# Kernel optimization log

Measured on AMD Instinct MI355X. Metric: run time of the kernel, lower is better.

## Reference

```python
import jax, jax.numpy as jnp
import numpy as np

N = 50000          # nodes
E_RAND = 800000    # random edges (avg degree 16)
IN, HID, HEADS, OUT = 256, 64, 4, 40
NEG_SLOPE = 0.2    # PyG GATConv default leaky_relu slope
BN_EPS = 1e-5


def setup_inputs() -> dict:
    key = jax.random.key(0)
    ks = jax.random.split(key, 24)
    x = jax.random.normal(ks[0], (N, IN), jnp.float32)
    ei = jax.random.randint(ks[1], (2, E_RAND), 0, N)
    loops = jnp.arange(N, dtype=ei.dtype)
    edge_index = jnp.concatenate([ei, jnp.stack([loops, loops])], axis=1)  # add self loops (PyG default)
    s = 0.1
    d = {
        "x": x,
        "edge_index": edge_index,
        "W0": jax.random.normal(ks[2], (IN, HEADS * HID), jnp.float32) * s,
        "a_src0": jax.random.normal(ks[3], (HEADS, HID), jnp.float32) * s,
        "a_dst0": jax.random.normal(ks[4], (HEADS, HID), jnp.float32) * s,
        "b0": jax.random.normal(ks[5], (HEADS * HID,), jnp.float32) * s,
        "bn0_g": jnp.ones((HEADS * HID,), jnp.float32),
        "bn0_b": jnp.zeros((HEADS * HID,), jnp.float32),
        "bn0_m": jax.random.normal(ks[6], (HEADS * HID,), jnp.float32) * s,
        "bn0_v": jax.random.uniform(ks[7], (HEADS * HID,), jnp.float32, 0.5, 1.5),
        "W1": jax.random.normal(ks[8], (HEADS * HID, HEADS * HID), jnp.float32) * s,
        "a_src1": jax.random.normal(ks[9], (HEADS, HID), jnp.float32) * s,
        "a_dst1": jax.random.normal(ks[10], (HEADS, HID), jnp.float32) * s,
        "b1": jax.random.normal(ks[11], (HEADS * HID,), jnp.float32) * s,
        "bn1_g": jnp.ones((HEADS * HID,), jnp.float32),
        "bn1_b": jnp.zeros((HEADS * HID,), jnp.float32),
        "bn1_m": jax.random.normal(ks[12], (HEADS * HID,), jnp.float32) * s,
        "bn1_v": jax.random.uniform(ks[13], (HEADS * HID,), jnp.float32, 0.5, 1.5),
        "W2": jax.random.normal(ks[14], (HEADS * HID, OUT), jnp.float32) * s,
        "a_src2": jax.random.normal(ks[15], (1, OUT), jnp.float32) * s,
        "a_dst2": jax.random.normal(ks[16], (1, OUT), jnp.float32) * s,
        "b2": jax.random.normal(ks[17], (OUT,), jnp.float32) * s,
    }
    return d


def gat_conv(x, edge_index, W, att_src, att_dst, heads, ch):
    """PyG GATConv (eval mode): gather -> leaky_relu attn -> segment softmax -> scatter add."""
    src, dst = edge_index[0], edge_index[1]
    h = (x @ W).reshape(-1, heads, ch)                       # [N,H,C]
    a_s = jnp.einsum('nhc,hc->nh', h, att_src)
    a_d = jnp.einsum('nhc,hc->nh', h, att_dst)
    e = jax.nn.leaky_relu(a_s[src] + a_d[dst], NEG_SLOPE)    # [E,H]
    m = jax.ops.segment_max(e, dst, num_segments=N)
    m = jax.lax.stop_gradient(jnp.where(jnp.isfinite(m), m, 0.0))
    p = jnp.exp(e - m[dst])
    denom = jax.ops.segment_sum(p, dst, num_segments=N)
    alpha = p / (denom[dst] + 1e-16)                         # [E,H]
    msg = h[src] * alpha[:, :, None]                         # [E,H,C]
    return jax.ops.segment_sum(msg, dst, num_segments=N)     # [N,H,C]


def _bn(h, g, b, m, v):
    return g * (h - m) * jax.lax.rsqrt(v + BN_EPS) + b


def reference(x, edge_index, W0, a_src0, a_dst0, b0, bn0_g, bn0_b, bn0_m, bn0_v,
              W1, a_src1, a_dst1, b1, bn1_g, bn1_b, bn1_m, bn1_v,
              W2, a_src2, a_dst2, b2):
    h = gat_conv(x, edge_index, W0, a_src0, a_dst0, HEADS, HID).reshape(N, HEADS * HID) + b0
    h = jax.nn.elu(_bn(h, bn0_g, bn0_b, bn0_m, bn0_v))
    h = gat_conv(h, edge_index, W1, a_src1, a_dst1, HEADS, HID).reshape(N, HEADS * HID) + b1
    h = jax.nn.elu(_bn(h, bn1_g, bn1_b, bn1_m, bn1_v))
    out = gat_conv(h, edge_index, W2, a_src2, a_dst2, 1, OUT).reshape(N, OUT) + b2
    return out
```

## Files before the change

kernel.cpp:

```cpp
#include <hip/hip_runtime.h>
#include <cstdint>
#include <cstddef>

constexpr int kN = 50000;
constexpr float kSlope = 0.2f;
constexpr float kBnEps = 1e-5f;

static inline int ceil_div(int a, int b) { return (a + b - 1) / b; }

typedef __attribute__((ext_vector_type(8))) _Float16 half8;
typedef __attribute__((ext_vector_type(8))) unsigned short ushortx8;
typedef __attribute__((ext_vector_type(4))) float f32x4;

__device__ inline unsigned short f2h_us(float f) {
  _Float16 h = (_Float16)f;
  return *(unsigned short*)&h;
}

__device__ inline void gload16(const void* g, void* l) {
  __builtin_amdgcn_global_load_lds((const __attribute__((address_space(1))) unsigned int*)g,
                                   (__attribute__((address_space(3))) unsigned int*)l, 16, 0, 0);
}


__global__ void k_prepw_degree(const int* __restrict__ dst, int* __restrict__ deg, int E,
                               const float* __restrict__ W0, unsigned short* __restrict__ Wt0,
                               const float* __restrict__ W1, unsigned short* __restrict__ Wt1,
                               const float* __restrict__ W2, unsigned short* __restrict__ Wt2) {
  const int tid = blockIdx.x * blockDim.x + threadIdx.x;
  const int nthr = gridDim.x * blockDim.x;
  for (int e = tid; e < E; e += nthr) atomicAdd(&deg[dst[e]], 1);
  const int S0 = 256 * 256, S1 = 256 * 256, S2 = 128 * 256;
  const int total = S0 + S1 + S2;
  for (int j = tid; j < total; j += nthr) {
    if (j < S0) {
      int nc = j >> 8, k = j & 255;
      Wt0[j] = f2h_us(W0[(size_t)k * 256 + nc]);
    } else if (j < S0 + S1) {
      int t = j - S0;
      int nc = t >> 8, k = t & 255;
      Wt1[t] = f2h_us(W1[(size_t)k * 256 + nc]);
    } else {
      int t = j - S0 - S1;
      int nc = t >> 8, k = t & 255;
      Wt2[t] = (nc < 40) ? f2h_us(W2[(size_t)k * 40 + nc]) : (unsigned short)0;
    }
  }
}


__global__ void k_scan1(const int* __restrict__ deg, int* __restrict__ rp,
                        int* __restrict__ bsum, int n) {
  __shared__ int sm[256];
  int i = blockIdx.x * 256 + threadIdx.x;
  int v = (i < n) ? deg[i] : 0;
  sm[threadIdx.x] = v;
  __syncthreads();
  for (int off = 1; off < 256; off <<= 1) {
    int t = (threadIdx.x >= off) ? sm[threadIdx.x - off] : 0;
    __syncthreads();
    sm[threadIdx.x] += t;
    __syncthreads();
  }
  if (i < n) rp[i + 1] = sm[threadIdx.x];
  if (threadIdx.x == 255) bsum[blockIdx.x] = sm[255];
}

__global__ void k_scan2(int* bsum, int nb) {
  __shared__ int sm[256];
  int v = (threadIdx.x < nb) ? bsum[threadIdx.x] : 0;
  sm[threadIdx.x] = v;
  __syncthreads();
  for (int off = 1; off < 256; off <<= 1) {
    int t = (threadIdx.x >= off) ? sm[threadIdx.x - off] : 0;
    __syncthreads();
    sm[threadIdx.x] += t;
    __syncthreads();
  }
  if (threadIdx.x < nb) bsum[threadIdx.x] = sm[threadIdx.x] - v;
}

__global__ void k_scan3(int* __restrict__ rp, const int* __restrict__ bsum, int n) {
  int i = blockIdx.x * 256 + threadIdx.x;
  if (i < n) rp[i + 1] += bsum[blockIdx.x];
  if (i == 0) rp[0] = 0;
}


template <bool AF32>
__device__ __forceinline__ void gemmN_body(int bx, const void* Av,
                                           const unsigned short* __restrict__ Bt,
                                           unsigned short* __restrict__ C,
                                           const float* __restrict__ asrc,
                                           const float* __restrict__ adst,
                                           float* __restrict__ a_s, float* __restrict__ a_d,
                                           int M) {
  constexpr int BM = 64, BK = 64, K = 256, NT = K / BK;
  __shared__ alignas(16) unsigned char AsRaw[BM * BK * (AF32 ? 4 : 2)];
  __shared__ alignas(16) unsigned short Bs[256 * BK];
  int tid = threadIdx.x;
  int wave = tid >> 6, lane = tid & 63;
  int quad = lane >> 4, l16 = lane & 15;
  int wn = wave * 64;
  int bm = bx * BM;
  f32x4 acc[4][4] = {};
  const float* Af = (const float*)Av;
  const unsigned short* Ah = (const unsigned short*)Av;

  for (int t = 0; t < NT; ++t) {
    int k0 = t * BK;
#pragma unroll
    for (int it = 0; it < 8; it++) {
      int u = wave * 8 + it;
      int brow = u * 8 + (lane >> 3);
      int bslot = (lane & 7) ^ (brow & 7);
      gload16(Bt + (size_t)brow * K + k0 + bslot * 8, (unsigned char*)Bs + u * 1024);
      if (AF32) {
        if (it < 4) {
          int ua = wave * 4 + it;
          int row = ua * 4 + (lane >> 4);
          int aslot = (lane & 15) ^ (row & 15);
          int gm = bm + row;
          if (gm >= M) gm = M - 1;
          gload16(Af + (size_t)gm * K + k0 + aslot * 4, AsRaw + ua * 1024);
        }
      } else {
        if (it < 2) {
          int ua = wave * 2 + it;
          int row = ua * 8 + (lane >> 3);
          int aslot = (lane & 7) ^ (row & 7);
          int gm = bm + row;
          if (gm >= M) gm = M - 1;
          gload16(Ah + (size_t)gm * K + k0 + aslot * 8, AsRaw + ua * 1024);
        }
      }
    }
    __syncthreads();
#pragma unroll
    for (int kk = 0; kk < 2; ++kk) {
      half8 af[4], bf[4];
#pragma unroll
      for (int i = 0; i < 4; i++) {
        int arow = i * 16 + l16;
        if (AF32) {
          const float4* As4 = (const float4*)AsRaw;
          int r15 = arow & 15;
          int sl = kk * 8 + quad * 2;
          float4 lo = As4[arow * 16 + (sl ^ r15)];
          float4 hi = As4[arow * 16 + ((sl + 1) ^ r15)];
          half8 a;
          a[0] = (_Float16)lo.x; a[1] = (_Float16)lo.y;
          a[2] = (_Float16)lo.z; a[3] = (_Float16)lo.w;
          a[4] = (_Float16)hi.x; a[5] = (_Float16)hi.y;
          a[6] = (_Float16)hi.z; a[7] = (_Float16)hi.w;
          af[i] = a;
        } else {
          int phys = (kk * 4 + quad) ^ (arow & 7);
          af[i] = *(const half8*)((const unsigned short*)AsRaw + arow * 64 + phys * 8);
        }
        int brow = wn + i * 16 + l16;
        int bphys = (kk * 4 + quad) ^ (brow & 7);
        bf[i] = *(const half8*)(Bs + (size_t)brow * 64 + bphys * 8);
      }
#pragma unroll
      for (int i = 0; i < 4; i++)
#pragma unroll
        for (int j = 0; j < 4; j++)
          acc[i][j] = __builtin_amdgcn_mfma_f32_16x16x32_f16(af[i], bf[j], acc[i][j], 0, 0, 0);
    }
    __syncthreads();
  }
#pragma unroll
  for (int i = 0; i < 4; i++) {
#pragma unroll
    for (int j = 0; j < 4; j++) {
      int col = wn + j * 16 + l16;
#pragma unroll
      for (int r = 0; r < 4; r++) {
        int row = bm + i * 16 + quad * 4 + r;
        if (row < M) C[(size_t)row * 256 + col] = f2h_us(acc[i][j][r]);
      }
    }
  }
  int ghead = wave;
  float asv[4], adv[4];
#pragma unroll
  for (int j = 0; j < 4; j++) {
    int col = wn + j * 16 + l16;
    asv[j] = asrc[col];
    adv[j] = adst[col];
  }
#pragma unroll
  for (int i = 0; i < 4; i++) {
#pragma unroll
    for (int r = 0; r < 4; r++) {
      float s = acc[i][0][r] * asv[0] + acc[i][1][r] * asv[1] + acc[i][2][r] * asv[2] +
                acc[i][3][r] * asv[3];
      float d = acc[i][0][r] * adv[0] + acc[i][1][r] * adv[1] + acc[i][2][r] * adv[2] +
                acc[i][3][r] * adv[3];
#pragma unroll
      for (int mask = 1; mask <= 8; mask <<= 1) {
        s += __shfl_xor(s, mask, 64);
        d += __shfl_xor(d, mask, 64);
      }
      if (l16 == 0) {
        int row = bm + i * 16 + quad * 4 + r;
        if (row < M) {
          a_s[row * 4 + ghead] = s;
          a_d[row * 4 + ghead] = d;
        }
      }
    }
  }
}

__global__ __launch_bounds__(256) void k_gemm0_scatter(
    const float* __restrict__ A, const unsigned short* __restrict__ Bt,
    unsigned short* __restrict__ C, const float* __restrict__ asrc,
    const float* __restrict__ adst, float* __restrict__ a_s, float* __restrict__ a_d, int M,
    int gemmBlocks, const int* __restrict__ src, const int* __restrict__ dst,
    const int* __restrict__ rp, int* __restrict__ cur, int* __restrict__ csr, int E) {
  if ((int)blockIdx.x < gemmBlocks) {
    gemmN_body<true>(blockIdx.x, A, Bt, C, asrc, adst, a_s, a_d, M);
  } else {
    int e = (blockIdx.x - gemmBlocks) * 256 + threadIdx.x;
    if (e < E) {
      int d = dst[e];
      int pos = rp[d] + atomicAdd(&cur[d], 1);
      csr[pos] = src[e];
    }
  }
}

__global__ __launch_bounds__(256) void k_gemmN_f16(
    const unsigned short* __restrict__ A, const unsigned short* __restrict__ Bt,
    unsigned short* __restrict__ C, const float* __restrict__ asrc,
    const float* __restrict__ adst, float* __restrict__ a_s, float* __restrict__ a_d, int M) {
  gemmN_body<false>(blockIdx.x, A, Bt, C, asrc, adst, a_s, a_d, M);
}


__global__ __launch_bounds__(256) void k_mfma_gemm(
    const unsigned short* __restrict__ A, const unsigned short* __restrict__ Bt,
    unsigned short* __restrict__ C, const float* __restrict__ asrc,
    const float* __restrict__ adst, float* __restrict__ a_s, float* __restrict__ a_d, int M,
    int K, int Nc, int ldc, int heads, int acols) {
  constexpr int BM = 128, BK = 32;
  __shared__ unsigned short As[BM * BK];
  __shared__ unsigned short Bs[BM * BK];
  int tid = threadIdx.x;
  int wave = tid >> 6, lane = tid & 63;
  int quad = lane >> 4, l16 = lane & 15;
  int wm = (wave & 1) * 64, wn = (wave >> 1) * 64;
  int bm = blockIdx.x * BM, bn = blockIdx.y * BM;
  int srow = lane >> 2;
  int spart = lane & 3;
  f32x4 acc[4][4] = {};
  for (int k0 = 0; k0 < K; k0 += BK) {
#pragma unroll
    for (int it = 0; it < 2; it++) {
      int chunk = wave * 2 + it;
      int row = chunk * 16 + srow;
      gload16(A + (size_t)(bm + row) * K + k0 + spart * 8, As + chunk * 512);
      gload16(Bt + (size_t)(bn + row) * K + k0 + spart * 8, Bs + chunk * 512);
    }
    __syncthreads();
    half8 af[4], bf[4];
#pragma unroll
    for (int i = 0; i < 4; i++) {
      af[i] = *(const half8*)(As + (wm + i * 16 + l16) * BK + quad * 8);
      bf[i] = *(const half8*)(Bs + (wn + i * 16 + l16) * BK + quad * 8);
    }
#pragma unroll
    for (int i = 0; i < 4; i++)
#pragma unroll
      for (int j = 0; j < 4; j++)
        acc[i][j] = __builtin_amdgcn_mfma_f32_16x16x32_f16(af[i], bf[j], acc[i][j], 0, 0, 0);
    __syncthreads();
  }
#pragma unroll
  for (int i = 0; i < 4; i++) {
#pragma unroll
    for (int j = 0; j < 4; j++) {
      int col = bn + wn + j * 16 + l16;
      if (col >= Nc) continue;
#pragma unroll
      for (int r = 0; r < 4; r++) {
        int row = bm + wm + i * 16 + quad * 4 + r;
        if (row < M) C[(size_t)row * ldc + col] = f2h_us(acc[i][j][r]);
      }
    }
  }
  int ghead = (bn + wn) >> 6;
  if (ghead < heads) {
    float asv[4], adv[4];
#pragma unroll
    for (int j = 0; j < 4; j++) {
      int col = bn + wn + j * 16 + l16;
      bool ok = col < acols;
      asv[j] = ok ? asrc[col] : 0.f;
      adv[j] = ok ? adst[col] : 0.f;
    }
#pragma unroll
    for (int i = 0; i < 4; i++) {
#pragma unroll
      for (int r = 0; r < 4; r++) {
        float s = acc[i][0][r] * asv[0] + acc[i][1][r] * asv[1] + acc[i][2][r] * asv[2] +
                  acc[i][3][r] * asv[3];
        float d = acc[i][0][r] * adv[0] + acc[i][1][r] * adv[1] + acc[i][2][r] * adv[2] +
                  acc[i][3][r] * adv[3];
#pragma unroll
        for (int mask = 1; mask <= 8; mask <<= 1) {
          s += __shfl_xor(s, mask, 64);
          d += __shfl_xor(d, mask, 64);
        }
        if (l16 == 0) {
          int row = bm + wm + i * 16 + quad * 4 + r;
          if (row < M) {
            a_s[row * heads + ghead] = s;
            a_d[row * heads + ghead] = d;
          }
        }
      }
    }
  }
}


__global__ __launch_bounds__(256) void k_attn_agg256(
    const int* __restrict__ rp, const int* __restrict__ csr, const _Float16* __restrict__ h,
    const float* __restrict__ a_s, const float* __restrict__ a_d, const float* __restrict__ bias,
    const float* __restrict__ bg, const float* __restrict__ bb, const float* __restrict__ bm,
    const float* __restrict__ bv, unsigned short* __restrict__ out, int n_nodes) {
  int wid = (blockIdx.x * blockDim.x + threadIdx.x) >> 6;
  int lane = threadIdx.x & 63;
  if (wid >= n_nodes) return;
  int n = wid;
  int beg = rp[n], end = rp[n + 1];
  int half = lane >> 5, l32 = lane & 31;
  int head = l32 >> 3;
  int c = l32 * 8;
  float ad = a_d[n * 4 + head];
  float acc[8] = {};
  float psum = 0.f;
  int e = beg;
  for (; e + 8 <= end; e += 8) {
    int s0 = csr[e + half];
    int s1 = csr[e + 2 + half];
    int s2 = csr[e + 4 + half];
    int s3 = csr[e + 6 + half];
    float x0 = a_s[s0 * 4 + head] + ad;
    float x1 = a_s[s1 * 4 + head] + ad;
    float x2 = a_s[s2 * 4 + head] + ad;
    float x3 = a_s[s3 * 4 + head] + ad;
    half8 v0 = *(const half8*)(h + (size_t)s0 * 256 + c);
    half8 v1 = *(const half8*)(h + (size_t)s1 * 256 + c);
    half8 v2 = *(const half8*)(h + (size_t)s2 * 256 + c);
    half8 v3 = *(const half8*)(h + (size_t)s3 * 256 + c);
    x0 = x0 > 0.f ? x0 : x0 * kSlope;
    x1 = x1 > 0.f ? x1 : x1 * kSlope;
    x2 = x2 > 0.f ? x2 : x2 * kSlope;
    x3 = x3 > 0.f ? x3 : x3 * kSlope;
    float p0 = __expf(x0), p1 = __expf(x1);
    float p2 = __expf(x2), p3 = __expf(x3);
    psum += (p0 + p1) + (p2 + p3);
#pragma unroll
    for (int j = 0; j < 8; j++) {
      acc[j] += (float)v0[j] * p0 + (float)v1[j] * p1;
      acc[j] += (float)v2[j] * p2 + (float)v3[j] * p3;
    }
  }
  for (; e + 2 <= end; e += 2) {
    int s0 = csr[e + half];
    float x0 = a_s[s0 * 4 + head] + ad;
    x0 = x0 > 0.f ? x0 : x0 * kSlope;
    float p0 = __expf(x0);
    psum += p0;
    half8 v0 = *(const half8*)(h + (size_t)s0 * 256 + c);
#pragma unroll
    for (int j = 0; j < 8; j++) acc[j] += (float)v0[j] * p0;
  }
  if (e < end && half == 0) {
    int s0 = csr[e];
    float x0 = a_s[s0 * 4 + head] + ad;
    x0 = x0 > 0.f ? x0 : x0 * kSlope;
    float p0 = __expf(x0);
    psum += p0;
    half8 v0 = *(const half8*)(h + (size_t)s0 * 256 + c);
#pragma unroll
    for (int j = 0; j < 8; j++) acc[j] += (float)v0[j] * p0;
  }
  psum += __shfl_xor(psum, 32, 64);
#pragma unroll
  for (int j = 0; j < 8; j++) acc[j] += __shfl_xor(acc[j], 32, 64);
  if (half == 0) {
    float rden = 1.f / (psum + 1e-16f);
    ushortx8 o;
#pragma unroll
    for (int j = 0; j < 8; j++) {
      float v = acc[j] * rden + bias[c + j];
      v = bg[c + j] * (v - bm[c + j]) * rsqrtf(bv[c + j] + kBnEps) + bb[c + j];
      v = v > 0.f ? v : (__expf(v) - 1.f);
      o[j] = f2h_us(v);
    }
    *(ushortx8*)(out + (size_t)n * 256 + c) = o;
  }
}


__global__ __launch_bounds__(256) void k_attn_agg40(
    const int* __restrict__ rp, const int* __restrict__ csr, const _Float16* __restrict__ h,
    const float* __restrict__ a_s, const float* __restrict__ a_d, const float* __restrict__ bias,
    float* __restrict__ out, int n_nodes) {
  int wid = (blockIdx.x * blockDim.x + threadIdx.x) >> 6;
  int lane = threadIdx.x & 63;
  if (wid >= n_nodes) return;
  int n = wid;
  int beg = rp[n], end = rp[n + 1];
  float ad = a_d[n];
  int grp = lane >> 3, l8 = lane & 7;
  int c = l8 * 8;
  bool act = l8 < 5;
  float acc[8] = {};
  float psum = 0.f;
  for (int base = beg; base < end; base += 16) {
    int e0 = base + grp;
    int e1 = base + 8 + grp;
    if (e0 < end) {
      int s = csr[e0];
      float x = a_s[s] + ad;
      x = x > 0.f ? x : x * kSlope;
      float p = __expf(x);
      psum += p;
      if (act) {
        half8 hv = *(const half8*)(h + (size_t)s * 40 + c);
#pragma unroll
        for (int j = 0; j < 8; j++) acc[j] += (float)hv[j] * p;
      }
    }
    if (e1 < end) {
      int s = csr[e1];
      float x = a_s[s] + ad;
      x = x > 0.f ? x : x * kSlope;
      float p = __expf(x);
      psum += p;
      if (act) {
        half8 hv = *(const half8*)(h + (size_t)s * 40 + c);
#pragma unroll
        for (int j = 0; j < 8; j++) acc[j] += (float)hv[j] * p;
      }
    }
  }
#pragma unroll
  for (int mask = 8; mask <= 32; mask <<= 1) psum += __shfl_xor(psum, mask, 64);
#pragma unroll
  for (int j = 0; j < 8; j++) {
#pragma unroll
    for (int mask = 8; mask <= 32; mask <<= 1) acc[j] += __shfl_xor(acc[j], mask, 64);
  }
  if (lane < 5) {
    float rden = 1.f / (psum + 1e-16f);
    float4 o0, o1;
    o0.x = acc[0] * rden + bias[c + 0];
    o0.y = acc[1] * rden + bias[c + 1];
    o0.z = acc[2] * rden + bias[c + 2];
    o0.w = acc[3] * rden + bias[c + 3];
    o1.x = acc[4] * rden + bias[c + 4];
    o1.y = acc[5] * rden + bias[c + 5];
    o1.z = acc[6] * rden + bias[c + 6];
    o1.w = acc[7] * rden + bias[c + 7];
    *(float4*)(out + (size_t)n * 40 + c) = o0;
    *(float4*)(out + (size_t)n * 40 + c + 4) = o1;
  }
}


extern "C" void kernel_launch(void* const* d_in, const int* in_sizes, int n_in, void* d_out,
                              int out_size, void* d_ws, size_t ws_size, hipStream_t stream) {
  const float* x = (const float*)d_in[0];
  const int* ei = (const int*)d_in[1];
  const float* W0 = (const float*)d_in[2];
  const float* as0 = (const float*)d_in[3];
  const float* ad0 = (const float*)d_in[4];
  const float* b0 = (const float*)d_in[5];
  const float* bg0 = (const float*)d_in[6];
  const float* bb0 = (const float*)d_in[7];
  const float* bm0 = (const float*)d_in[8];
  const float* bv0 = (const float*)d_in[9];
  const float* W1 = (const float*)d_in[10];
  const float* as1 = (const float*)d_in[11];
  const float* ad1 = (const float*)d_in[12];
  const float* b1 = (const float*)d_in[13];
  const float* bg1 = (const float*)d_in[14];
  const float* bb1 = (const float*)d_in[15];
  const float* bm1 = (const float*)d_in[16];
  const float* bv1 = (const float*)d_in[17];
  const float* W2 = (const float*)d_in[18];
  const float* as2 = (const float*)d_in[19];
  const float* ad2 = (const float*)d_in[20];
  const float* b2 = (const float*)d_in[21];
  float* out = (float*)d_out;

  const int E = in_sizes[1] / 2;
  const int* srcIdx = ei;
  const int* dstIdx = ei + E;

  char* p = (char*)d_ws;
  auto alloc = [&](size_t bytes) -> void* {
    void* r = (void*)p;
    p += (bytes + 255) & ~(size_t)255;
    return r;
  };
  int* rp = (int*)alloc((kN + 1) * sizeof(int));
  int* degcur = (int*)alloc((size_t)2 * kN * sizeof(int));
  int* deg = degcur;
  int* cur = degcur + kN;
  int* bsum = (int*)alloc(256 * sizeof(int));
  int* csr = (int*)alloc((size_t)E * sizeof(int));
  float* a_s = (float*)alloc((size_t)kN * 4 * sizeof(float));
  float* a_d = (float*)alloc((size_t)kN * 4 * sizeof(float));
  unsigned short* h16 = (unsigned short*)alloc((size_t)kN * 256 * 2);
  unsigned short* act16 = (unsigned short*)alloc((size_t)kN * 256 * 2);
  unsigned short* Wt0 = (unsigned short*)alloc((size_t)256 * 256 * 2);
  unsigned short* Wt1 = (unsigned short*)alloc((size_t)256 * 256 * 2);
  unsigned short* Wt2 = (unsigned short*)alloc((size_t)128 * 256 * 2);

  const int nb = ceil_div(kN, 256);

  hipMemsetAsync(degcur, 0, (size_t)2 * kN * sizeof(int), stream);
  k_prepw_degree<<<1024, 256, 0, stream>>>(dstIdx, deg, E, W0, Wt0, W1, Wt1, W2, Wt2);
  k_scan1<<<nb, 256, 0, stream>>>(deg, rp, bsum, kN);
  k_scan2<<<1, 256, 0, stream>>>(bsum, nb);
  k_scan3<<<nb, 256, 0, stream>>>(rp, bsum, kN);

  const int gemmBlocks = ceil_div(kN, 64);
  const int sblocks = ceil_div(E, 256);
  k_gemm0_scatter<<<gemmBlocks + sblocks, 256, 0, stream>>>(
      x, Wt0, h16, as0, ad0, a_s, a_d, kN, gemmBlocks, srcIdx, dstIdx, rp, cur, csr, E);

  int wpn_blocks = ceil_div(kN, 4);
  dim3 gg2(ceil_div(kN, 128), 1);

  k_attn_agg256<<<wpn_blocks, 256, 0, stream>>>(rp, csr, (const _Float16*)h16, a_s, a_d, b0, bg0,
                                                bb0, bm0, bv0, act16, kN);

  k_gemmN_f16<<<gemmBlocks, 256, 0, stream>>>(act16, Wt1, h16, as1, ad1, a_s, a_d, kN);
  k_attn_agg256<<<wpn_blocks, 256, 0, stream>>>(rp, csr, (const _Float16*)h16, a_s, a_d, b1, bg1,
                                                bb1, bm1, bv1, act16, kN);

  k_mfma_gemm<<<gg2, 256, 0, stream>>>(act16, Wt2, h16, as2, ad2, a_s, a_d, kN, 256, 40, 40, 1,
                                       40);
  k_attn_agg40<<<wpn_blocks, 256, 0, stream>>>(rp, csr, (const _Float16*)h16, a_s, a_d, b2, out,
                                               kN);
}
```

Before: 418.9 us.

## Specialize final-layer GEMM for 40 output columns with swizzled LDS tiles

Replaces the generic 128x128-tile MFMA GEMM for the last layer with a dedicated kernel using 64-row tiles, 48 padded output columns and a 64-wide K step. The old kernel computed a 128-wide column tile of which only 40 columns were used. The new one cuts that wasted MFMA work and LDS traffic and launches more blocks. It also XOR-swizzles the LDS layout to avoid bank conflicts and clamps out-of-range rows instead of reading past the end of A. The cost is a hardcoded K=256 and 40-column output shape.

```diff
diff --git a/kernel.cpp b/kernel.cpp
--- a/kernel.cpp
+++ b/kernel.cpp
@@ -240,88 +240,78 @@
 }
 
 
-__global__ __launch_bounds__(256) void k_mfma_gemm(
+__global__ __launch_bounds__(256) void k_gemm40(
     const unsigned short* __restrict__ A, const unsigned short* __restrict__ Bt,
     unsigned short* __restrict__ C, const float* __restrict__ asrc,
-    const float* __restrict__ adst, float* __restrict__ a_s, float* __restrict__ a_d, int M,
-    int K, int Nc, int ldc, int heads, int acols) {
-  constexpr int BM = 128, BK = 32;
-  __shared__ unsigned short As[BM * BK];
-  __shared__ unsigned short Bs[BM * BK];
+    const float* __restrict__ adst, float* __restrict__ a_s, float* __restrict__ a_d, int M) {
+  constexpr int BM = 64, BK = 64, K = 256, NT = K / BK;
+  __shared__ alignas(16) unsigned short As[BM * BK];
+  __shared__ alignas(16) unsigned short Bs[48 * BK];
   int tid = threadIdx.x;
   int wave = tid >> 6, lane = tid & 63;
   int quad = lane >> 4, l16 = lane & 15;
-  int wm = (wave & 1) * 64, wn = (wave >> 1) * 64;
-  int bm = blockIdx.x * BM, bn = blockIdx.y * BM;
-  int srow = lane >> 2;
-  int spart = lane & 3;
-  f32x4 acc[4][4] = {};
-  for (int k0 = 0; k0 < K; k0 += BK) {
+  int bm = blockIdx.x * BM;
+  f32x4 acc[3] = {};
+  for (int t = 0; t < NT; ++t) {
+    int k0 = t * BK;
 #pragma unroll
     for (int it = 0; it < 2; it++) {
-      int chunk = wave * 2 + it;
-      int row = chunk * 16 + srow;
-      gload16(A + (size_t)(bm + row) * K + k0 + spart * 8, As + chunk * 512);
-      gload16(Bt + (size_t)(bn + row) * K + k0 + spart * 8, Bs + chunk * 512);
-    }
-    __syncthreads();
-    half8 af[4], bf[4];
-#pragma unroll
-    for (int i = 0; i < 4; i++) {
-      af[i] = *(const half8*)(As + (wm + i * 16 + l16) * BK + quad * 8);
-      bf[i] = *(const half8*)(Bs + (wn + i * 16 + l16) * BK + quad * 8);
-    }
-#pragma unroll
-    for (int i = 0; i < 4; i++)
-#pragma unroll
-      for (int j = 0; j < 4; j++)
-        acc[i][j] = __builtin_amdgcn_mfma_f32_16x16x32_f16(af[i], bf[j], acc[i][j], 0, 0, 0);
-    __syncthreads();
-  }
-#pragma unroll
-  for (int i = 0; i < 4; i++) {
-#pragma unroll
-    for (int j = 0; j < 4; j++) {
-      int col = bn + wn + j * 16 + l16;
-      if (col >= Nc) continue;
-#pragma unroll
-      for (int r = 0; r < 4; r++) {
-        int row = bm + wm + i * 16 + quad * 4 + r;
-        if (row < M) C[(size_t)row * ldc + col] = f2h_us(acc[i][j][r]);
-      }
-    }
-  }
-  int ghead = (bn + wn) >> 6;
-  if (ghead < heads) {
-    float asv[4], adv[4];
-#pragma unroll
-    for (int j = 0; j < 4; j++) {
-      int col = bn + wn + j * 16 + l16;
-      bool ok = col < acols;
-      asv[j] = ok ? asrc[col] : 0.f;
-      adv[j] = ok ? adst[col] : 0.f;
-    }
-#pragma unroll
-    for (int i = 0; i < 4; i++) {
-#pragma unroll
-      for (int r = 0; r < 4; r++) {
-        float s = acc[i][0][r] * asv[0] + acc[i][1][r] * asv[1] + acc[i][2][r] * asv[2] +
-                  acc[i][3][r] * asv[3];
-        float d = acc[i][0][r] * adv[0] + acc[i][1][r] * adv[1] + acc[i][2][r] * adv[2] +
-                  acc[i][3][r] * adv[3];
-#pragma unroll
-        for (int mask = 1; mask <= 8; mask <<= 1) {
-          s += __shfl_xor(s, mask, 64);
-          d += __shfl_xor(d, mask, 64);
-        }
-        if (l16 == 0) {
-          int row = bm + wm + i * 16 + quad * 4 + r;
-          if (row < M) {
-            a_s[row * heads + ghead] = s;
-            a_d[row * heads + ghead] = d;
-          }
-        }
-      }
+      int ua = wave * 2 + it;
+      int arow = ua * 8 + (lane >> 3);
+      int aslot = (lane & 7) ^ (arow & 7);
+      int gm = bm + arow;
+      if (gm >= M) gm = M - 1;
+      gload16(A + (size_t)gm * K + k0 + aslot * 8, (unsigned char*)As + ua * 1024);
+      int ub = wave * 2 + it;
+      if (ub < 6) {
+        int brow = ub * 8 + (lane >> 3);
+        int bslot = (lane & 7) ^ (brow & 7);
+        gload16(Bt + (size_t)brow * K + k0 + bslot * 8, (unsigned char*)Bs + ub * 1024);
+      }
+    }
+    __syncthreads();
+#pragma unroll
+    for (int kk = 0; kk < 2; ++kk) {
+      int arow = wave * 16 + l16;
+      int aphys = (kk * 4 + quad) ^ (arow & 7);
+      half8 af = *(const half8*)(As + (size_t)arow * 64 + aphys * 8);
+#pragma unroll
+      for (int j = 0; j < 3; j++) {
+        int brow = j * 16 + l16;
+        int bphys = (kk * 4 + quad) ^ (brow & 7);
+        half8 bf = *(const half8*)(Bs + (size_t)brow * 64 + bphys * 8);
+        acc[j] = __builtin_amdgcn_mfma_f32_16x16x32_f16(af, bf, acc[j], 0, 0, 0);
+      }
+    }
+    __syncthreads();
+  }
+  float asv[3], adv[3];
+#pragma unroll
+  for (int j = 0; j < 3; j++) {
+    int col = j * 16 + l16;
+    bool ok = col < 40;
+    asv[j] = ok ? asrc[col] : 0.f;
+    adv[j] = ok ? adst[col] : 0.f;
+  }
+#pragma unroll
+  for (int r = 0; r < 4; r++) {
+    int row = bm + wave * 16 + quad * 4 + r;
+    bool rok = row < M;
+#pragma unroll
+    for (int j = 0; j < 3; j++) {
+      int col = j * 16 + l16;
+      if (rok && col < 40) C[(size_t)row * 40 + col] = f2h_us(acc[j][r]);
+    }
+    float s = acc[0][r] * asv[0] + acc[1][r] * asv[1] + acc[2][r] * asv[2];
+    float d = acc[0][r] * adv[0] + acc[1][r] * adv[1] + acc[2][r] * adv[2];
+#pragma unroll
+    for (int mask = 1; mask <= 8; mask <<= 1) {
+      s += __shfl_xor(s, mask, 64);
+      d += __shfl_xor(d, mask, 64);
+    }
+    if (l16 == 0 && rok) {
+      a_s[row] = s;
+      a_d[row] = d;
     }
   }
 }
@@ -539,7 +529,6 @@
       x, Wt0, h16, as0, ad0, a_s, a_d, kN, gemmBlocks, srcIdx, dstIdx, rp, cur, csr, E);
 
   int wpn_blocks = ceil_div(kN, 4);
-  dim3 gg2(ceil_div(kN, 128), 1);
 
   k_attn_agg256<<<wpn_blocks, 256, 0, stream>>>(rp, csr, (const _Float16*)h16, a_s, a_d, b0, bg0,
                                                 bb0, bm0, bv0, act16, kN);
@@ -548,8 +537,7 @@
   k_attn_agg256<<<wpn_blocks, 256, 0, stream>>>(rp, csr, (const _Float16*)h16, a_s, a_d, b1, bg1,
                                                 bb1, bm1, bv1, act16, kN);
 
-  k_mfma_gemm<<<gg2, 256, 0, stream>>>(act16, Wt2, h16, as2, ad2, a_s, a_d, kN, 256, 40, 40, 1,
-                                       40);
+  k_gemm40<<<gemmBlocks, 256, 0, stream>>>(act16, Wt2, h16, as2, ad2, a_s, a_d, kN);
   k_attn_agg40<<<wpn_blocks, 256, 0, stream>>>(rp, csr, (const _Float16*)h16, a_s, a_d, b2, out,
                                                kN);
 }
```

New measurement: 407.9 us. 1.03x faster.
